# Performance work log

Measured on AMD Instinct MI355X. Metric: run time of the kernel, lower is better.

The kernel has to match this reference:

```python
import jax, jax.numpy as jnp
import numpy as np

S_SCALE = 64.0   # arcface scale
MARGIN = 0.5     # arcface additive angular margin
EMB = 512
NUM_CLASSES = 100000
BATCH = 512


def setup_inputs() -> dict:
    key = jax.random.key(0)
    k1, k2, k3, k4 = jax.random.split(key, 4)
    # xavier_uniform for [num_classes, emb]
    limit = float(np.sqrt(6.0 / (NUM_CLASSES + EMB)))
    weight = jax.random.uniform(k1, (NUM_CLASSES, EMB), jnp.float32, -limit, limit)
    fc_weight = jax.random.uniform(k2, (NUM_CLASSES, EMB), jnp.float32, -limit, limit)
    local_embeddings = jax.random.normal(k3, (BATCH, EMB), jnp.float32)
    local_labels = jax.random.randint(k4, (BATCH,), 0, NUM_CLASSES, jnp.int64)
    return {
        "local_embeddings": local_embeddings,
        "weight": weight,
        "fc_weight": fc_weight,
        "local_labels": local_labels,
        "epoch": 40,
    }


def _l2norm(x, eps=1e-12):
    return x / jnp.maximum(jnp.linalg.norm(x, axis=-1, keepdims=True), eps)


def _arcface(logits, labels):
    # insightface ArcFace: replace target cosine with cos(theta + m), then scale by s
    rows = jnp.arange(logits.shape[0])
    target = logits[rows, labels]
    sin = jnp.sqrt(jnp.maximum(1.0 - target * target, 0.0))
    cos_m, sin_m = jnp.cos(MARGIN), jnp.sin(MARGIN)
    with_margin = target * cos_m - sin * sin_m            # cos(theta + m)
    # safeguard: only apply when theta + m <= pi  (target > cos(pi - m))
    threshold = jnp.cos(jnp.pi - MARGIN)
    mm = jnp.sin(jnp.pi - MARGIN) * MARGIN
    new_target = jnp.where(target > threshold, with_margin, target - mm)
    logits = logits.at[rows, labels].set(new_target)
    return logits * S_SCALE


def _ce(logits, labels):
    rows = jnp.arange(logits.shape[0])
    logp = jax.nn.log_softmax(logits, axis=-1)
    return -jnp.mean(logp[rows, labels])


def reference(local_embeddings, weight, fc_weight, local_labels, epoch):
    labels = local_labels.astype(jnp.int32)
    # margin branch: normalize both sides, cosine logits, arcface margin, CE
    norm_emb = _l2norm(local_embeddings)
    norm_w = _l2norm(weight)
    logits = norm_emb @ norm_w.T                   # [B, num_classes]
    logits = _arcface(logits, labels)
    margin_loss = _ce(logits, labels)
    # plain CE branch on raw linear
    ce_logits = local_embeddings @ fc_weight.T     # [B, num_classes]
    ce_loss = _ce(ce_logits, labels)
    if epoch <= 30:
        return ce_loss + 0.0 * margin_loss
    else:
        return 0.0 * ce_loss + margin_loss
```

## Files before the change

kernel.cpp:

```cpp
#include <hip/hip_runtime.h>

typedef __bf16 bf16x8 __attribute__((ext_vector_type(8)));
typedef float floatx4 __attribute__((ext_vector_type(4)));
typedef unsigned short ushortx8 __attribute__((ext_vector_type(8)));
typedef unsigned short ushort_t;

#define NC      100000
#define NCP     100096
#define EMBD    512
#define BATCH   512
#define BM      128
#define BN      128
#define BK      32
#define NCH     782

#define COS_M   0.8775825618903728f
#define SIN_M   0.479425538604203f
#define THRESH  (-0.8775825618903728f)
#define MM_C    0.2397127693021015f

__device__ __forceinline__ ushort_t f2bf(float f) {
  __bf16 h = (__bf16)f;
  return __builtin_bit_cast(ushort_t, h);
}

#define GLOAD16(g, l) __builtin_amdgcn_global_load_lds( \
    (const __attribute__((address_space(1))) void*)(g), \
    (__attribute__((address_space(3))) void*)(l), 16, 0, 0)

__global__ void detect64_k(const int* __restrict__ labels, int* __restrict__ flag) {
  __shared__ int nz;
  if (threadIdx.x == 0) nz = 0;
  __syncthreads();
  if (labels[2 * threadIdx.x + 1] != 0) atomicAdd(&nz, 1);
  __syncthreads();
  if (threadIdx.x == 0) flag[0] = (nz == 0) ? 1 : 0;
}

__global__ __launch_bounds__(256) void prep_a_k(
    const float* __restrict__ emb, const int* __restrict__ epoch,
    ushort_t* __restrict__ Abf) {
  const bool mm = (*epoch > 30);
  const int w = threadIdx.x >> 6, lane = threadIdx.x & 63;
  const int row = blockIdx.x * 4 + w;
  const float* src = emb + (size_t)row * EMBD + lane * 8;
  float4 a = *(const float4*)src;
  float4 b = *(const float4*)(src + 4);
  float ss = a.x*a.x + a.y*a.y + a.z*a.z + a.w*a.w
           + b.x*b.x + b.y*b.y + b.z*b.z + b.w*b.w;
  #pragma unroll
  for (int off = 32; off; off >>= 1) ss += __shfl_xor(ss, off, 64);
  const float inv = mm ? (1.0f / fmaxf(sqrtf(ss), 1e-12f)) : 1.0f;
  ushortx8 o;
  o[0] = f2bf(a.x*inv); o[1] = f2bf(a.y*inv); o[2] = f2bf(a.z*inv); o[3] = f2bf(a.w*inv);
  o[4] = f2bf(b.x*inv); o[5] = f2bf(b.y*inv); o[6] = f2bf(b.z*inv); o[7] = f2bf(b.w*inv);
  *(ushortx8*)(Abf + (size_t)row * EMBD + lane * 8) = o;
}

__global__ __launch_bounds__(256) void prep_w_k(
    const float* __restrict__ weight, const float* __restrict__ fcw,
    const int* __restrict__ epoch, ushort_t* __restrict__ Wbf) {
  const bool mm = (*epoch > 30);
  const float* W = mm ? weight : fcw;
  const int w = threadIdx.x >> 6, lane = threadIdx.x & 63;
  const int row = blockIdx.x * 4 + w;
  if (row >= NCP) return;
  ushort_t* dst = Wbf + (size_t)row * EMBD + lane * 8;
  if (row >= NC) {
    ushortx8 z = (ushortx8)0;
    *(ushortx8*)dst = z;
    return;
  }
  const float* src = W + (size_t)row * EMBD + lane * 8;
  float4 a = *(const float4*)src;
  float4 b = *(const float4*)(src + 4);
  float ss = a.x*a.x + a.y*a.y + a.z*a.z + a.w*a.w
           + b.x*b.x + b.y*b.y + b.z*b.z + b.w*b.w;
  #pragma unroll
  for (int off = 32; off; off >>= 1) ss += __shfl_xor(ss, off, 64);
  const float inv = mm ? (1.0f / fmaxf(sqrtf(ss), 1e-12f)) : 1.0f;
  ushortx8 o;
  o[0] = f2bf(a.x*inv); o[1] = f2bf(a.y*inv); o[2] = f2bf(a.z*inv); o[3] = f2bf(a.w*inv);
  o[4] = f2bf(b.x*inv); o[5] = f2bf(b.y*inv); o[6] = f2bf(b.z*inv); o[7] = f2bf(b.w*inv);
  *(ushortx8*)dst = o;
}

__global__ __launch_bounds__(256) void target_k(
    const float* __restrict__ emb, const float* __restrict__ weight,
    const float* __restrict__ fcw, const int* __restrict__ labels,
    const int* __restrict__ epoch, const int* __restrict__ flag64,
    float* __restrict__ tsc) {
  const bool mm = (*epoch > 30);
  const float* W = mm ? weight : fcw;
  const int w = threadIdx.x >> 6, lane = threadIdx.x & 63;
  const int b = blockIdx.x * 4 + w;
  const int lab = (*flag64) ? labels[2 * b] : labels[b];
  const float* er = emb + (size_t)b * EMBD + lane * 8;
  const float* wr = W + (size_t)lab * EMBD + lane * 8;
  float4 e0 = *(const float4*)er,       e1 = *(const float4*)(er + 4);
  float4 w0 = *(const float4*)wr,       w1 = *(const float4*)(wr + 4);
  float dot = e0.x*w0.x + e0.y*w0.y + e0.z*w0.z + e0.w*w0.w
            + e1.x*w1.x + e1.y*w1.y + e1.z*w1.z + e1.w*w1.w;
  float ssa = e0.x*e0.x + e0.y*e0.y + e0.z*e0.z + e0.w*e0.w
            + e1.x*e1.x + e1.y*e1.y + e1.z*e1.z + e1.w*e1.w;
  float ssw = w0.x*w0.x + w0.y*w0.y + w0.z*w0.z + w0.w*w0.w
            + w1.x*w1.x + w1.y*w1.y + w1.z*w1.z + w1.w*w1.w;
  #pragma unroll
  for (int off = 32; off; off >>= 1) {
    dot += __shfl_xor(dot, off, 64);
    ssa += __shfl_xor(ssa, off, 64);
    ssw += __shfl_xor(ssw, off, 64);
  }
  if (lane == 0) {
    if (mm) {
      float cosv = dot / (fmaxf(sqrtf(ssa), 1e-12f) * fmaxf(sqrtf(ssw), 1e-12f));
      float sinv = sqrtf(fmaxf(1.0f - cosv * cosv, 0.0f));
      float wmarg = cosv * COS_M - sinv * SIN_M;
      float nt = (cosv > THRESH) ? wmarg : (cosv - MM_C);
      tsc[b] = 64.0f * nt;
    } else {
      tsc[b] = dot;
    }
  }
}

__global__ __launch_bounds__(256, 2) void gemm_fused_k(
    const ushort_t* __restrict__ Abf, const ushort_t* __restrict__ Wbf,
    const float* __restrict__ tsc, const int* __restrict__ labels,
    const int* __restrict__ flag64, const int* __restrict__ epoch,
    float2* __restrict__ partials) {
  const bool mm = (*epoch > 30);
  const float scale = mm ? 64.0f : 1.0f;

  __shared__ ushort_t As[BM * BK];
  __shared__ ushort_t Bs[BN * BK];
  __shared__ float redM[BM * 2];
  __shared__ float redS[BM * 2];
  __shared__ float tscS[BM];
  __shared__ int   labS[BM];

  const int tid  = threadIdx.x;
  const int lane = tid & 63;
  const int w    = tid >> 6;
  const int wm   = (w >> 1) * 64;
  const int wn   = (w & 1) * 64;
  const int bm   = blockIdx.x & 3;
  const int bn   = blockIdx.x >> 2;
  const int m0   = bm * BM;
  const int n0   = bn * BN;

  if (tid < BM) {
    tscS[tid] = tsc[m0 + tid];
    labS[tid] = (*flag64) ? labels[2 * (m0 + tid)] : labels[m0 + tid];
  }

  floatx4 acc[4][4];
  #pragma unroll
  for (int i = 0; i < 4; i++)
    #pragma unroll
    for (int j = 0; j < 4; j++) acc[i][j] = (floatx4){0.f, 0.f, 0.f, 0.f};

  const int seg0 = 2 * w, seg1 = 2 * w + 1;
  const int r_in = lane >> 2;
  const int k_in = (lane & 3) * 8;
  const ushort_t* gA0 = Abf + (size_t)(m0 + seg0 * 16 + r_in) * EMBD + k_in;
  const ushort_t* gA1 = Abf + (size_t)(m0 + seg1 * 16 + r_in) * EMBD + k_in;
  const ushort_t* gB0 = Wbf + (size_t)(n0 + seg0 * 16 + r_in) * EMBD + k_in;
  const ushort_t* gB1 = Wbf + (size_t)(n0 + seg1 * 16 + r_in) * EMBD + k_in;
  ushort_t* lA0 = &As[seg0 * 512 + lane * 8];
  ushort_t* lA1 = &As[seg1 * 512 + lane * 8];
  ushort_t* lB0 = &Bs[seg0 * 512 + lane * 8];
  ushort_t* lB1 = &Bs[seg1 * 512 + lane * 8];

  const int koff = (lane >> 4) * 8;
  const int rsel = lane & 15;

  for (int kt = 0; kt < EMBD / BK; ++kt) {
    GLOAD16(gA0 + kt * BK, lA0);
    GLOAD16(gA1 + kt * BK, lA1);
    GLOAD16(gB0 + kt * BK, lB0);
    GLOAD16(gB1 + kt * BK, lB1);
    __syncthreads();

    bf16x8 af[4], bfv[4];
    #pragma unroll
    for (int mi = 0; mi < 4; mi++)
      af[mi] = *(const bf16x8*)&As[(wm + mi * 16 + rsel) * BK + koff];
    #pragma unroll
    for (int ni = 0; ni < 4; ni++)
      bfv[ni] = *(const bf16x8*)&Bs[(wn + ni * 16 + rsel) * BK + koff];
    #pragma unroll
    for (int mi = 0; mi < 4; mi++)
      #pragma unroll
      for (int ni = 0; ni < 4; ni++)
        acc[mi][ni] = __builtin_amdgcn_mfma_f32_16x16x32_bf16(
            af[mi], bfv[ni], acc[mi][ni], 0, 0, 0);
    __syncthreads();
  }

  const int colq = lane & 15;
  const int rowq = lane >> 4;
  #pragma unroll
  for (int mi = 0; mi < 4; mi++) {
    #pragma unroll
    for (int r = 0; r < 4; r++) {
      const int rl = wm + mi * 16 + rowq * 4 + r;
      const int lab = labS[rl];
      const float tv = tscS[rl];
      float v[4];
      #pragma unroll
      for (int ni = 0; ni < 4; ni++) {
        const int cg = n0 + wn + ni * 16 + colq;
        float x = acc[mi][ni][r] * scale;
        if (cg >= NC) x = -1e30f;
        else if (cg == lab) x = tv;
        v[ni] = x;
      }
      float mx = fmaxf(fmaxf(v[0], v[1]), fmaxf(v[2], v[3]));
      #pragma unroll
      for (int off = 1; off < 16; off <<= 1) mx = fmaxf(mx, __shfl_xor(mx, off, 64));
      float s = __expf(v[0] - mx) + __expf(v[1] - mx)
              + __expf(v[2] - mx) + __expf(v[3] - mx);
      #pragma unroll
      for (int off = 1; off < 16; off <<= 1) s += __shfl_xor(s, off, 64);
      if (colq == 0) { redM[rl * 2 + (w & 1)] = mx; redS[rl * 2 + (w & 1)] = s; }
    }
  }
  __syncthreads();
  if (tid < BM) {
    const float ma = redM[tid * 2], mb = redM[tid * 2 + 1];
    const float sa = redS[tid * 2], sb = redS[tid * 2 + 1];
    const float M = fmaxf(ma, mb);
    const float S = sa * __expf(ma - M) + sb * __expf(mb - M);
    partials[(size_t)(m0 + tid) * NCH + bn] = make_float2(M, S);
  }
}

__global__ __launch_bounds__(256) void rowmerge_k(
    const float2* __restrict__ partials, const float* __restrict__ tsc,
    float* __restrict__ loss_row) {
  const int row = blockIdx.x;
  const int tid = threadIdx.x;
  float M = -1e30f, S = 0.0f;
  for (int j = tid; j < NCH; j += 256) {
    const float2 p = partials[(size_t)row * NCH + j];
    if (p.x > M) { S = S * __expf(M - p.x) + p.y; M = p.x; }
    else         { S += p.y * __expf(p.x - M); }
  }
  __shared__ float sm[256], sv[256];
  sm[tid] = M; sv[tid] = S;
  __syncthreads();
  for (int st = 128; st > 0; st >>= 1) {
    if (tid < st) {
      const float m2 = sm[tid + st], s2 = sv[tid + st];
      const float m1 = sm[tid],      s1 = sv[tid];
      const float Mn = fmaxf(m1, m2);
      sv[tid] = s1 * __expf(m1 - Mn) + s2 * __expf(m2 - Mn);
      sm[tid] = Mn;
    }
    __syncthreads();
  }
  if (tid == 0) loss_row[row] = (sm[0] + __logf(sv[0])) - tsc[row];
}

__global__ __launch_bounds__(512) void finalsum_k(
    const float* __restrict__ loss_row, float* __restrict__ out) {
  const int tid = threadIdx.x;
  __shared__ float buf[512];
  buf[tid] = loss_row[tid];
  __syncthreads();
  for (int st = 256; st > 0; st >>= 1) {
    if (tid < st) buf[tid] += buf[tid + st];
    __syncthreads();
  }
  if (tid == 0) out[0] = buf[0] / 512.0f;
}

extern "C" void kernel_launch(void* const* d_in, const int* in_sizes, int n_in,
                              void* d_out, int out_size, void* d_ws, size_t ws_size,
                              hipStream_t stream) {
  const float* emb    = (const float*)d_in[0];
  const float* weight = (const float*)d_in[1];
  const float* fcw    = (const float*)d_in[2];
  const int*   labels = (const int*)d_in[3];
  const int*   epoch  = (const int*)d_in[4];
  float* out = (float*)d_out;

  char* ws = (char*)d_ws;
  size_t off = 0;
  ushort_t* Abf = (ushort_t*)(ws + off); off += (size_t)BATCH * EMBD * 2;
  ushort_t* Wbf = (ushort_t*)(ws + off); off += (size_t)NCP * EMBD * 2;
  float* tsc       = (float*)(ws + off); off += BATCH * 4;
  float2* partials = (float2*)(ws + off); off += (size_t)BATCH * NCH * 8;
  float* loss_row  = (float*)(ws + off); off += BATCH * 4;
  int* flag64      = (int*)(ws + off);   off += 256;

  detect64_k<<<1, 256, 0, stream>>>(labels, flag64);
  prep_a_k <<<BATCH / 4, 256, 0, stream>>>(emb, epoch, Abf);
  prep_w_k <<<NCP / 4, 256, 0, stream>>>(weight, fcw, epoch, Wbf);
  target_k <<<BATCH / 4, 256, 0, stream>>>(emb, weight, fcw, labels, epoch, flag64, tsc);
  gemm_fused_k<<<4 * NCH, 256, 0, stream>>>(Abf, Wbf, tsc, labels, flag64, epoch, partials);
  rowmerge_k<<<BATCH, 256, 0, stream>>>(partials, tsc, loss_row);
  finalsum_k<<<1, 512, 0, stream>>>(loss_row, out);
}
```

Baseline: 481.5 us.

## Enlarge GEMM M-tile to 256, group N-tiles, and fuse small prep and reduction kernels

The fused GEMM tile grows from 128x128 to 256x128, with each wave owning 64 rows across all 128 columns, so each weight tile is loaded by only two blocks instead of four. Blocks are grouped so neighbouring blocks share W tiles through L2. Per-row partials are written straight from registers, which removes the shared-memory cross-wave merge. Label detection, A normalisation and target-logit computation move into a single prep kernel, and the final mean becomes an atomicAdd inside rowmerge, which cuts the launch count. The 128 fp32 accumulators per thread raise register pressure under launch_bounds(256,2), and the atomic summation order is nondeterministic.

```diff
diff --git a/kernel.cpp b/kernel.cpp
--- a/kernel.cpp
+++ b/kernel.cpp
@@ -9,7 +9,7 @@
 #define NCP     100096
 #define EMBD    512
 #define BATCH   512
-#define BM      128
+#define BM      256
 #define BN      128
 #define BK      32
 #define NCH     782
@@ -28,33 +28,59 @@
     (const __attribute__((address_space(1))) void*)(g), \
     (__attribute__((address_space(3))) void*)(l), 16, 0, 0)
 
-__global__ void detect64_k(const int* __restrict__ labels, int* __restrict__ flag) {
-  __shared__ int nz;
-  if (threadIdx.x == 0) nz = 0;
-  __syncthreads();
-  if (labels[2 * threadIdx.x + 1] != 0) atomicAdd(&nz, 1);
-  __syncthreads();
-  if (threadIdx.x == 0) flag[0] = (nz == 0) ? 1 : 0;
-}
-
-__global__ __launch_bounds__(256) void prep_a_k(
-    const float* __restrict__ emb, const int* __restrict__ epoch,
-    ushort_t* __restrict__ Abf) {
+__global__ __launch_bounds__(256) void prep_small_k(
+    const float* __restrict__ emb, const float* __restrict__ weight,
+    const float* __restrict__ fcw, const int* __restrict__ labels,
+    const int* __restrict__ epoch, ushort_t* __restrict__ Abf,
+    float* __restrict__ tsc, int* __restrict__ lab32,
+    float* __restrict__ out) {
   const bool mm = (*epoch > 30);
-  const int w = threadIdx.x >> 6, lane = threadIdx.x & 63;
+  const int tid = threadIdx.x;
+  const int pred = (labels[2 * tid + 1] != 0) ? 1 : 0;
+  const bool is64 = (__syncthreads_or(pred) == 0);
+
+  const int w = tid >> 6, lane = tid & 63;
   const int row = blockIdx.x * 4 + w;
-  const float* src = emb + (size_t)row * EMBD + lane * 8;
-  float4 a = *(const float4*)src;
-  float4 b = *(const float4*)(src + 4);
-  float ss = a.x*a.x + a.y*a.y + a.z*a.z + a.w*a.w
-           + b.x*b.x + b.y*b.y + b.z*b.z + b.w*b.w;
-  #pragma unroll
-  for (int off = 32; off; off >>= 1) ss += __shfl_xor(ss, off, 64);
-  const float inv = mm ? (1.0f / fmaxf(sqrtf(ss), 1e-12f)) : 1.0f;
+  const int lab = is64 ? labels[2 * row] : labels[row];
+  const float* W = mm ? weight : fcw;
+
+  const float* er = emb + (size_t)row * EMBD + lane * 8;
+  const float* wr = W + (size_t)lab * EMBD + lane * 8;
+  float4 e0 = *(const float4*)er,  e1 = *(const float4*)(er + 4);
+  float4 w0 = *(const float4*)wr,  w1 = *(const float4*)(wr + 4);
+  float dot = e0.x*w0.x + e0.y*w0.y + e0.z*w0.z + e0.w*w0.w
+            + e1.x*w1.x + e1.y*w1.y + e1.z*w1.z + e1.w*w1.w;
+  float ssa = e0.x*e0.x + e0.y*e0.y + e0.z*e0.z + e0.w*e0.w
+            + e1.x*e1.x + e1.y*e1.y + e1.z*e1.z + e1.w*e1.w;
+  float ssw = w0.x*w0.x + w0.y*w0.y + w0.z*w0.z + w0.w*w0.w
+            + w1.x*w1.x + w1.y*w1.y + w1.z*w1.z + w1.w*w1.w;
+  #pragma unroll
+  for (int off = 32; off; off >>= 1) {
+    dot += __shfl_xor(dot, off, 64);
+    ssa += __shfl_xor(ssa, off, 64);
+    ssw += __shfl_xor(ssw, off, 64);
+  }
+  const float inva = mm ? (1.0f / fmaxf(sqrtf(ssa), 1e-12f)) : 1.0f;
   ushortx8 o;
-  o[0] = f2bf(a.x*inv); o[1] = f2bf(a.y*inv); o[2] = f2bf(a.z*inv); o[3] = f2bf(a.w*inv);
-  o[4] = f2bf(b.x*inv); o[5] = f2bf(b.y*inv); o[6] = f2bf(b.z*inv); o[7] = f2bf(b.w*inv);
+  o[0] = f2bf(e0.x*inva); o[1] = f2bf(e0.y*inva); o[2] = f2bf(e0.z*inva); o[3] = f2bf(e0.w*inva);
+  o[4] = f2bf(e1.x*inva); o[5] = f2bf(e1.y*inva); o[6] = f2bf(e1.z*inva); o[7] = f2bf(e1.w*inva);
   *(ushortx8*)(Abf + (size_t)row * EMBD + lane * 8) = o;
+
+  if (lane == 0) {
+    lab32[row] = lab;
+    float tv;
+    if (mm) {
+      float cosv = dot / (fmaxf(sqrtf(ssa), 1e-12f) * fmaxf(sqrtf(ssw), 1e-12f));
+      float sinv = sqrtf(fmaxf(1.0f - cosv * cosv, 0.0f));
+      float wmarg = cosv * COS_M - sinv * SIN_M;
+      float nt = (cosv > THRESH) ? wmarg : (cosv - MM_C);
+      tv = 64.0f * nt;
+    } else {
+      tv = dot;
+    }
+    tsc[row] = tv;
+  }
+  if (blockIdx.x == 0 && tid == 0) out[0] = 0.0f;
 }
 
 __global__ __launch_bounds__(256) void prep_w_k(
@@ -64,11 +90,9 @@
   const float* W = mm ? weight : fcw;
   const int w = threadIdx.x >> 6, lane = threadIdx.x & 63;
   const int row = blockIdx.x * 4 + w;
-  if (row >= NCP) return;
   ushort_t* dst = Wbf + (size_t)row * EMBD + lane * 8;
   if (row >= NC) {
-    ushortx8 z = (ushortx8)0;
-    *(ushortx8*)dst = z;
+    *(ushortx8*)dst = (ushortx8)0;
     return;
   }
   const float* src = W + (size_t)row * EMBD + lane * 8;
@@ -85,116 +109,79 @@
   *(ushortx8*)dst = o;
 }
 
-__global__ __launch_bounds__(256) void target_k(
-    const float* __restrict__ emb, const float* __restrict__ weight,
-    const float* __restrict__ fcw, const int* __restrict__ labels,
-    const int* __restrict__ epoch, const int* __restrict__ flag64,
-    float* __restrict__ tsc) {
-  const bool mm = (*epoch > 30);
-  const float* W = mm ? weight : fcw;
-  const int w = threadIdx.x >> 6, lane = threadIdx.x & 63;
-  const int b = blockIdx.x * 4 + w;
-  const int lab = (*flag64) ? labels[2 * b] : labels[b];
-  const float* er = emb + (size_t)b * EMBD + lane * 8;
-  const float* wr = W + (size_t)lab * EMBD + lane * 8;
-  float4 e0 = *(const float4*)er,       e1 = *(const float4*)(er + 4);
-  float4 w0 = *(const float4*)wr,       w1 = *(const float4*)(wr + 4);
-  float dot = e0.x*w0.x + e0.y*w0.y + e0.z*w0.z + e0.w*w0.w
-            + e1.x*w1.x + e1.y*w1.y + e1.z*w1.z + e1.w*w1.w;
-  float ssa = e0.x*e0.x + e0.y*e0.y + e0.z*e0.z + e0.w*e0.w
-            + e1.x*e1.x + e1.y*e1.y + e1.z*e1.z + e1.w*e1.w;
-  float ssw = w0.x*w0.x + w0.y*w0.y + w0.z*w0.z + w0.w*w0.w
-            + w1.x*w1.x + w1.y*w1.y + w1.z*w1.z + w1.w*w1.w;
-  #pragma unroll
-  for (int off = 32; off; off >>= 1) {
-    dot += __shfl_xor(dot, off, 64);
-    ssa += __shfl_xor(ssa, off, 64);
-    ssw += __shfl_xor(ssw, off, 64);
-  }
-  if (lane == 0) {
-    if (mm) {
-      float cosv = dot / (fmaxf(sqrtf(ssa), 1e-12f) * fmaxf(sqrtf(ssw), 1e-12f));
-      float sinv = sqrtf(fmaxf(1.0f - cosv * cosv, 0.0f));
-      float wmarg = cosv * COS_M - sinv * SIN_M;
-      float nt = (cosv > THRESH) ? wmarg : (cosv - MM_C);
-      tsc[b] = 64.0f * nt;
-    } else {
-      tsc[b] = dot;
-    }
-  }
-}
-
 __global__ __launch_bounds__(256, 2) void gemm_fused_k(
     const ushort_t* __restrict__ Abf, const ushort_t* __restrict__ Wbf,
-    const float* __restrict__ tsc, const int* __restrict__ labels,
-    const int* __restrict__ flag64, const int* __restrict__ epoch,
-    float2* __restrict__ partials) {
+    const float* __restrict__ tsc, const int* __restrict__ lab32,
+    const int* __restrict__ epoch, float2* __restrict__ partials) {
+  const int g = blockIdx.x >> 4, t = blockIdx.x & 15;
+  const int bn = g * 8 + (t & 7);
+  const int bm = t >> 3;
+  if (bn >= NCH) return;
+
   const bool mm = (*epoch > 30);
   const float scale = mm ? 64.0f : 1.0f;
 
   __shared__ ushort_t As[BM * BK];
   __shared__ ushort_t Bs[BN * BK];
-  __shared__ float redM[BM * 2];
-  __shared__ float redS[BM * 2];
   __shared__ float tscS[BM];
   __shared__ int   labS[BM];
 
   const int tid  = threadIdx.x;
   const int lane = tid & 63;
   const int w    = tid >> 6;
-  const int wm   = (w >> 1) * 64;
-  const int wn   = (w & 1) * 64;
-  const int bm   = blockIdx.x & 3;
-  const int bn   = blockIdx.x >> 2;
+  const int wm   = w * 64;
   const int m0   = bm * BM;
   const int n0   = bn * BN;
 
-  if (tid < BM) {
-    tscS[tid] = tsc[m0 + tid];
-    labS[tid] = (*flag64) ? labels[2 * (m0 + tid)] : labels[m0 + tid];
-  }
-
-  floatx4 acc[4][4];
+  tscS[tid] = tsc[m0 + tid];
+  labS[tid] = lab32[m0 + tid];
+
+  floatx4 acc[4][8];
   #pragma unroll
   for (int i = 0; i < 4; i++)
     #pragma unroll
-    for (int j = 0; j < 4; j++) acc[i][j] = (floatx4){0.f, 0.f, 0.f, 0.f};
-
-  const int seg0 = 2 * w, seg1 = 2 * w + 1;
+    for (int j = 0; j < 8; j++) acc[i][j] = (floatx4){0.f, 0.f, 0.f, 0.f};
+
   const int r_in = lane >> 2;
   const int k_in = (lane & 3) * 8;
-  const ushort_t* gA0 = Abf + (size_t)(m0 + seg0 * 16 + r_in) * EMBD + k_in;
-  const ushort_t* gA1 = Abf + (size_t)(m0 + seg1 * 16 + r_in) * EMBD + k_in;
-  const ushort_t* gB0 = Wbf + (size_t)(n0 + seg0 * 16 + r_in) * EMBD + k_in;
-  const ushort_t* gB1 = Wbf + (size_t)(n0 + seg1 * 16 + r_in) * EMBD + k_in;
-  ushort_t* lA0 = &As[seg0 * 512 + lane * 8];
-  ushort_t* lA1 = &As[seg1 * 512 + lane * 8];
-  ushort_t* lB0 = &Bs[seg0 * 512 + lane * 8];
-  ushort_t* lB1 = &Bs[seg1 * 512 + lane * 8];
+  const ushort_t* gA[4];
+  ushort_t* lA[4];
+  #pragma unroll
+  for (int s = 0; s < 4; s++) {
+    gA[s] = Abf + (size_t)(m0 + wm + s * 16 + r_in) * EMBD + k_in;
+    lA[s] = &As[(wm + s * 16) * BK + lane * 8];
+  }
+  const ushort_t* gB[2];
+  ushort_t* lB[2];
+  #pragma unroll
+  for (int s = 0; s < 2; s++) {
+    gB[s] = Wbf + (size_t)(n0 + w * 32 + s * 16 + r_in) * EMBD + k_in;
+    lB[s] = &Bs[(w * 32 + s * 16) * BK + lane * 8];
+  }
 
   const int koff = (lane >> 4) * 8;
   const int rsel = lane & 15;
 
   for (int kt = 0; kt < EMBD / BK; ++kt) {
-    GLOAD16(gA0 + kt * BK, lA0);
-    GLOAD16(gA1 + kt * BK, lA1);
-    GLOAD16(gB0 + kt * BK, lB0);
-    GLOAD16(gB1 + kt * BK, lB1);
+    #pragma unroll
+    for (int s = 0; s < 4; s++) GLOAD16(gA[s] + kt * BK, lA[s]);
+    #pragma unroll
+    for (int s = 0; s < 2; s++) GLOAD16(gB[s] + kt * BK, lB[s]);
     __syncthreads();
 
-    bf16x8 af[4], bfv[4];
+    bf16x8 af[4], bv[8];
     #pragma unroll
     for (int mi = 0; mi < 4; mi++)
       af[mi] = *(const bf16x8*)&As[(wm + mi * 16 + rsel) * BK + koff];
     #pragma unroll
-    for (int ni = 0; ni < 4; ni++)
-      bfv[ni] = *(const bf16x8*)&Bs[(wn + ni * 16 + rsel) * BK + koff];
+    for (int ni = 0; ni < 8; ni++)
+      bv[ni] = *(const bf16x8*)&Bs[(ni * 16 + rsel) * BK + koff];
     #pragma unroll
     for (int mi = 0; mi < 4; mi++)
       #pragma unroll
-      for (int ni = 0; ni < 4; ni++)
+      for (int ni = 0; ni < 8; ni++)
         acc[mi][ni] = __builtin_amdgcn_mfma_f32_16x16x32_bf16(
-            af[mi], bfv[ni], acc[mi][ni], 0, 0, 0);
+            af[mi], bv[ni], acc[mi][ni], 0, 0, 0);
     __syncthreads();
   }
 
@@ -207,38 +194,34 @@
       const int rl = wm + mi * 16 + rowq * 4 + r;
       const int lab = labS[rl];
       const float tv = tscS[rl];
-      float v[4];
-      #pragma unroll
-      for (int ni = 0; ni < 4; ni++) {
-        const int cg = n0 + wn + ni * 16 + colq;
+      float v[8];
+      #pragma unroll
+      for (int ni = 0; ni < 8; ni++) {
+        const int cg = n0 + ni * 16 + colq;
         float x = acc[mi][ni][r] * scale;
         if (cg >= NC) x = -1e30f;
         else if (cg == lab) x = tv;
         v[ni] = x;
       }
-      float mx = fmaxf(fmaxf(v[0], v[1]), fmaxf(v[2], v[3]));
+      float mx = v[0];
+      #pragma unroll
+      for (int ni = 1; ni < 8; ni++) mx = fmaxf(mx, v[ni]);
       #pragma unroll
       for (int off = 1; off < 16; off <<= 1) mx = fmaxf(mx, __shfl_xor(mx, off, 64));
-      float s = __expf(v[0] - mx) + __expf(v[1] - mx)
-              + __expf(v[2] - mx) + __expf(v[3] - mx);
+      float s = 0.0f;
+      #pragma unroll
+      for (int ni = 0; ni < 8; ni++) s += __expf(v[ni] - mx);
       #pragma unroll
       for (int off = 1; off < 16; off <<= 1) s += __shfl_xor(s, off, 64);
-      if (colq == 0) { redM[rl * 2 + (w & 1)] = mx; redS[rl * 2 + (w & 1)] = s; }
+      if (colq == 0)
+        partials[(size_t)(m0 + rl) * NCH + bn] = make_float2(mx, s);
     }
-  }
-  __syncthreads();
-  if (tid < BM) {
-    const float ma = redM[tid * 2], mb = redM[tid * 2 + 1];
-    const float sa = redS[tid * 2], sb = redS[tid * 2 + 1];
-    const float M = fmaxf(ma, mb);
-    const float S = sa * __expf(ma - M) + sb * __expf(mb - M);
-    partials[(size_t)(m0 + tid) * NCH + bn] = make_float2(M, S);
   }
 }
 
 __global__ __launch_bounds__(256) void rowmerge_k(
     const float2* __restrict__ partials, const float* __restrict__ tsc,
-    float* __restrict__ loss_row) {
+    float* __restrict__ out) {
   const int row = blockIdx.x;
   const int tid = threadIdx.x;
   float M = -1e30f, S = 0.0f;
@@ -260,20 +243,10 @@
     }
     __syncthreads();
   }
-  if (tid == 0) loss_row[row] = (sm[0] + __logf(sv[0])) - tsc[row];
-}
-
-__global__ __launch_bounds__(512) void finalsum_k(
-    const float* __restrict__ loss_row, float* __restrict__ out) {
-  const int tid = threadIdx.x;
-  __shared__ float buf[512];
-  buf[tid] = loss_row[tid];
-  __syncthreads();
-  for (int st = 256; st > 0; st >>= 1) {
-    if (tid < st) buf[tid] += buf[tid + st];
-    __syncthreads();
-  }
-  if (tid == 0) out[0] = buf[0] / 512.0f;
+  if (tid == 0) {
+    const float loss = (sm[0] + __logf(sv[0])) - tsc[row];
+    atomicAdd(out, loss * (1.0f / 512.0f));
+  }
 }
 
 extern "C" void kernel_launch(void* const* d_in, const int* in_sizes, int n_in,
@@ -291,15 +264,12 @@
   ushort_t* Abf = (ushort_t*)(ws + off); off += (size_t)BATCH * EMBD * 2;
   ushort_t* Wbf = (ushort_t*)(ws + off); off += (size_t)NCP * EMBD * 2;
   float* tsc       = (float*)(ws + off); off += BATCH * 4;
+  int* lab32       = (int*)(ws + off);   off += BATCH * 4;
   float2* partials = (float2*)(ws + off); off += (size_t)BATCH * NCH * 8;
-  float* loss_row  = (float*)(ws + off); off += BATCH * 4;
-  int* flag64      = (int*)(ws + off);   off += 256;
-
-  detect64_k<<<1, 256, 0, stream>>>(labels, flag64);
-  prep_a_k <<<BATCH / 4, 256, 0, stream>>>(emb, epoch, Abf);
-  prep_w_k <<<NCP / 4, 256, 0, stream>>>(weight, fcw, epoch, Wbf);
-  target_k <<<BATCH / 4, 256, 0, stream>>>(emb, weight, fcw, labels, epoch, flag64, tsc);
-  gemm_fused_k<<<4 * NCH, 256, 0, stream>>>(Abf, Wbf, tsc, labels, flag64, epoch, partials);
-  rowmerge_k<<<BATCH, 256, 0, stream>>>(partials, tsc, loss_row);
-  finalsum_k<<<1, 512, 0, stream>>>(loss_row, out);
-}
+
+  prep_small_k<<<BATCH / 4, 256, 0, stream>>>(emb, weight, fcw, labels, epoch,
+                                              Abf, tsc, lab32, out);
+  prep_w_k<<<NCP / 4, 256, 0, stream>>>(weight, fcw, epoch, Wbf);
+  gemm_fused_k<<<98 * 16, 256, 0, stream>>>(Abf, Wbf, tsc, lab32, epoch, partials);
+  rowmerge_k<<<BATCH, 256, 0, stream>>>(partials, tsc, out);
+}
```

New measurement: 473.5 us. About the same (-1.7%).
